# Kernel optimization log

Hardware: AMD Instinct MI355X
Metric: run time of the kernel (lower is better)

Reference implementation:

```python
import jax, jax.numpy as jnp
import numpy as np

N, E = 50000, 500000          # nodes, edges
IN_DIM, HID, OUT = 512, 256, 64  # hidden_dims = [in_dim, num_hidden, out_dim]


def setup_inputs() -> dict:
    key = jax.random.key(0)
    ks = jax.random.split(key, 6)
    features = jax.random.normal(ks[0], (N, IN_DIM), jnp.float32)
    edge_index = jax.random.randint(ks[1], (2, E), 0, N, jnp.int32)  # [src; dst]
    s1 = 1.0 / np.sqrt(IN_DIM)
    s2 = 1.0 / np.sqrt(HID)
    # torch.nn.Linear convention: weight shape (out, in), y = x @ W.T
    W1 = jax.random.uniform(ks[2], (HID, IN_DIM), jnp.float32, -s1, s1)
    W2 = jax.random.uniform(ks[3], (OUT, HID), jnp.float32, -s2, s2)
    att_src = jax.random.normal(ks[4], (HID,), jnp.float32) * 0.1
    att_dst = jax.random.normal(ks[5], (HID,), jnp.float32) * 0.1
    return dict(features=features, W1=W1, W2=W2,
                att_src=att_src, att_dst=att_dst, edge_index=edge_index)


def _gat_propagate(h, a_src, a_dst, src, dst, n):
    """STAGATE GATConv propagate: sigmoid attention logits + PyG segment softmax
    over destination nodes, then scatter-sum of weighted source features."""
    a = jax.nn.sigmoid(a_src[src] + a_dst[dst])          # [E] edge logits
    mx = jax.ops.segment_max(a, dst, num_segments=n)     # [N] per-dest max
    mx = jnp.where(jnp.isfinite(mx), mx, 0.0)            # empty segments -> 0
    e = jnp.exp(a - mx[dst])                             # [E]
    denom = jax.ops.segment_sum(e, dst, num_segments=n)  # [N]
    w = e / (denom[dst] + 1e-16)                         # [E] softmax weights
    return jax.ops.segment_sum(h[src] * w[:, None], dst, num_segments=n)


def reference(features, W1, W2, att_src, att_dst, edge_index):
    src, dst = edge_index[0], edge_index[1]
    n = features.shape[0]
    # conv1: attention=True (heads=1, concat=False)
    h1p = features @ W1.T                 # [N, HID]
    a_src = h1p @ att_src                 # [N] node-level alpha_src
    a_dst = h1p @ att_dst                 # [N] node-level alpha_dst
    h1 = jax.nn.elu(_gat_propagate(h1p, a_src, a_dst, src, dst, n))
    # conv2: attention=False -> linear only
    h2 = h1 @ W2.T                        # [N, OUT]
    # conv3: weight tied to W2.T, tied_attention = conv1's node alphas
    h3p = h2 @ W2                         # [N, HID]
    h3 = jax.nn.elu(_gat_propagate(h3p, a_src, a_dst, src, dst, n))
    # conv4: attention=False, weight tied to W1.T
    h4 = h3 @ W1                          # [N, IN_DIM]
    return h2, h4
```

## Files before the change

### kernel.cpp

```cpp
#include <hip/hip_runtime.h>
#include <hip/hip_bf16.h>

typedef unsigned short u16;
typedef unsigned int   u32;

#define N_NODES 50000
#define N_EDGES 500000
#define IN_DIM  512
#define HID     256
#define OUT_DIM 64

typedef __bf16 bf16x8 __attribute__((ext_vector_type(8)));
typedef float  f32x4  __attribute__((ext_vector_type(4)));

#define GLOBAL_AS __attribute__((address_space(1)))
#define LDS_AS    __attribute__((address_space(3)))

__device__ __forceinline__ float bf2f(u16 u) {
  union { u32 i; float f; } x; x.i = ((u32)u) << 16; return x.f;
}
__device__ __forceinline__ u16 f2bf(float f) {
  union { float f; u32 i; } x; x.f = f;
  u32 r = x.i + 0x7FFFu + ((x.i >> 16) & 1u);
  return (u16)(r >> 16);
}
__device__ __forceinline__ u32 pkbf(float a, float b) {
  return (u32)f2bf(a) | ((u32)f2bf(b) << 16);
}
__device__ __forceinline__ float lo2f(u32 w) {
  union { u32 i; float f; } x; x.i = w << 16; return x.f;
}
__device__ __forceinline__ float hi2f(u32 w) {
  union { u32 i; float f; } x; x.i = w & 0xFFFF0000u; return x.f;
}

__global__ void detect_dtype(const u32* __restrict__ feat, int* __restrict__ flag) {
  __shared__ int s[256];
  int t = threadIdx.x;
  int hits = 0;
  for (int i = t; i < 1024; i += 256) {
    u32 e = (feat[i] >> 7) & 0xFF;
    hits += (e >= 100 && e <= 140) ? 1 : 0;
  }
  s[t] = hits;
  __syncthreads();
  for (int o = 128; o > 0; o >>= 1) {
    if (t < o) s[t] += s[t + o];
    __syncthreads();
  }
  if (t == 0) *flag = (s[0] > 716) ? 1 : 0;
}

__global__ void prep(const void* __restrict__ W1r, const void* __restrict__ W2r,
                     const void* __restrict__ atsr, const void* __restrict__ atdr,
                     u16* __restrict__ W1b, u16* __restrict__ W2b,
                     u16* __restrict__ attsb, u16* __restrict__ attdb,
                     u16* __restrict__ W1T, u16* __restrict__ W2T,
                     const int* __restrict__ flag) {
  const int fv = *flag;
  int i = blockIdx.x * 256 + threadIdx.x;
  int stride = gridDim.x * 256;
  const int NW1 = HID * IN_DIM;
  const int NW2 = OUT_DIM * HID;
  for (int j = i; j < NW1; j += stride) {
    u16 v = fv ? ((const u16*)W1r)[j] : f2bf(((const float*)W1r)[j]);
    W1b[j] = v;
    int r = j >> 9, c = j & 511;
    W1T[c * HID + r] = v;
  }
  for (int j = i; j < NW2; j += stride) {
    u16 v = fv ? ((const u16*)W2r)[j] : f2bf(((const float*)W2r)[j]);
    W2b[j] = v;
    int r = j >> 8, c = j & 255;
    W2T[c * OUT_DIM + r] = v;
  }
  if (blockIdx.x == 0 && threadIdx.x < HID) {
    int t = threadIdx.x;
    attsb[t] = fv ? ((const u16*)atsr)[t] : f2bf(((const float*)atsr)[t]);
    attdb[t] = fv ? ((const u16*)atdr)[t] : f2bf(((const float*)atdr)[t]);
  }
}

__device__ __forceinline__ void glds16(const u16* g, __bf16* l) {
  __builtin_amdgcn_global_load_lds((const GLOBAL_AS u32*)g, (LDS_AS u32*)l, 16, 0, 0);
}

template <int MODE, int ABF16>
__global__ __launch_bounds__(256) void gemm128(const u16* __restrict__ A,
                                               const float* __restrict__ Af32,
                                               const u16* __restrict__ B,
                                               u16* __restrict__ Cb,
                                               void* __restrict__ outbase,
                                               size_t out_off,
                                               const u16* __restrict__ attsb,
                                               const u16* __restrict__ attdb,
                                               float* __restrict__ a_s,
                                               float* __restrict__ a_d,
                                               const int* __restrict__ flag,
                                               int M, int N, int K) {
  __shared__ __bf16 As[64 * 64];
  __shared__ __bf16 Bs[128 * 64];
  __shared__ float as_l[128];
  __shared__ float ad_l[128];

  const int fv = *flag;
  if (MODE == 3 && ABF16 != fv) return;

  const int tid  = threadIdx.x;
  const int wave = tid >> 6;
  const int lane = tid & 63;
  const int m0   = blockIdx.x * 64;
  const int n0   = blockIdx.y * 128;
  const int wm   = (wave >> 1) * 32;
  const int wn   = (wave & 1) * 64;
  const int quad = lane >> 4;
  const int l16  = lane & 15;

  if (MODE == 3 && tid < 128) {
    as_l[tid] = bf2f(attsb[n0 + tid]);
    ad_l[tid] = bf2f(attdb[n0 + tid]);
  }

  const int r8 = lane >> 3;
  const int sg = (lane & 7) ^ r8;

  const u16* bp[4];
#pragma unroll
  for (int l = 0; l < 4; ++l) {
    int br = n0 + l * 32 + wave * 8 + r8;
    bp[l] = B + (size_t)br * K + sg * 8;
  }

  const u16* ap[2];
  if (ABF16) {
#pragma unroll
    for (int l = 0; l < 2; ++l) {
      int ar = m0 + l * 32 + wave * 8 + r8;
      if (ar >= M) ar = M - 1;
      ap[l] = A + (size_t)ar * K + sg * 8;
    }
  }
  const float* afp = nullptr;
  const int rr = tid >> 2, hh = tid & 3;
  if (!ABF16) {
    int ar = m0 + rr;
    if (ar >= M) ar = M - 1;
    afp = Af32 + (size_t)ar * K + hh * 16;
  }

  f32x4 acc[2][4];
#pragma unroll
  for (int i = 0; i < 2; ++i)
#pragma unroll
    for (int j = 0; j < 4; ++j) acc[i][j] = (f32x4)0.f;

  float4 fa[4];
  if (!ABF16) {
#pragma unroll
    for (int c = 0; c < 4; ++c) fa[c] = *(const float4*)(afp + 4 * c);
  }

  for (int k0 = 0; k0 < K; k0 += 64) {
    if (ABF16) {
      __syncthreads();
#pragma unroll
      for (int l = 0; l < 2; ++l)
        glds16(ap[l] + k0, As + (l * 32 + wave * 8) * 64);
#pragma unroll
      for (int l = 0; l < 4; ++l)
        glds16(bp[l] + k0, Bs + (l * 32 + wave * 8) * 64);
      __syncthreads();
    } else {
      __builtin_amdgcn_s_barrier();
      __builtin_amdgcn_sched_barrier(0);
#pragma unroll
      for (int l = 0; l < 4; ++l)
        glds16(bp[l] + k0, Bs + (l * 32 + wave * 8) * 64);
      __builtin_amdgcn_sched_barrier(0);
#pragma unroll
      for (int j = 0; j < 2; ++j) {
        int phys = ((hh * 2 + j) ^ (rr & 7)) * 8;
        uint4 o;
        o.x = pkbf(fa[2 * j].x, fa[2 * j].y);
        o.y = pkbf(fa[2 * j].z, fa[2 * j].w);
        o.z = pkbf(fa[2 * j + 1].x, fa[2 * j + 1].y);
        o.w = pkbf(fa[2 * j + 1].z, fa[2 * j + 1].w);
        *(uint4*)&As[rr * 64 + phys] = o;
      }
      __builtin_amdgcn_sched_barrier(0);
      if (k0 + 64 < K) {
#pragma unroll
        for (int c = 0; c < 4; ++c)
          fa[c] = *(const float4*)(afp + k0 + 64 + 4 * c);
        __builtin_amdgcn_sched_barrier(0);
        asm volatile("s_waitcnt vmcnt(4) lgkmcnt(0)" ::: "memory");
      } else {
        asm volatile("s_waitcnt vmcnt(0) lgkmcnt(0)" ::: "memory");
      }
      __builtin_amdgcn_sched_barrier(0);
      __builtin_amdgcn_s_barrier();
      __builtin_amdgcn_sched_barrier(0);
    }

    bf16x8 af[2][2], bfr[4][2];
#pragma unroll
    for (int ks = 0; ks < 2; ++ks) {
#pragma unroll
      for (int mi = 0; mi < 2; ++mi)
        af[mi][ks] = *(const bf16x8*)&As[(wm + mi * 16 + l16) * 64 +
                                         (((ks * 4 + quad) ^ (l16 & 7)) * 8)];
#pragma unroll
      for (int ni = 0; ni < 4; ++ni)
        bfr[ni][ks] = *(const bf16x8*)&Bs[(wn + ni * 16 + l16) * 64 +
                                          (((ks * 4 + quad) ^ (l16 & 7)) * 8)];
    }
#pragma unroll
    for (int ks = 0; ks < 2; ++ks)
#pragma unroll
      for (int mi = 0; mi < 2; ++mi)
#pragma unroll
        for (int ni = 0; ni < 4; ++ni)
          acc[mi][ni] = __builtin_amdgcn_mfma_f32_16x16x32_bf16(
              af[mi][ks], bfr[ni][ks], acc[mi][ni], 0, 0, 0);
  }

  if (MODE == 3) {
    __syncthreads();
#pragma unroll
    for (int mi = 0; mi < 2; ++mi)
#pragma unroll
      for (int r = 0; r < 4; ++r) {
        float ps = 0.f, pd = 0.f;
#pragma unroll
        for (int ni = 0; ni < 4; ++ni) {
          int c = wn + ni * 16 + l16;
          ps += acc[mi][ni][r] * as_l[c];
          pd += acc[mi][ni][r] * ad_l[c];
        }
#pragma unroll
        for (int o = 1; o < 16; o <<= 1) {
          ps += __shfl_xor(ps, o);
          pd += __shfl_xor(pd, o);
        }
        int gr = m0 + wm + mi * 16 + quad * 4 + r;
        if (l16 == 0 && gr < M) {
          atomicAdd(&a_s[gr], ps);
          atomicAdd(&a_d[gr], pd);
        }
      }
  }

#pragma unroll
  for (int mi = 0; mi < 2; ++mi)
#pragma unroll
    for (int ni = 0; ni < 4; ++ni)
#pragma unroll
      for (int r = 0; r < 4; ++r) {
        int gr = m0 + wm + mi * 16 + quad * 4 + r;
        int gc = n0 + wn + ni * 16 + l16;
        if (gr < M) {
          float  v   = acc[mi][ni][r];
          size_t idx = (size_t)gr * N + gc;
          if (MODE == 1) {
            if (fv) ((u16*)outbase)[out_off + idx] = f2bf(v);
            else    ((float*)outbase)[out_off + idx] = v;
          } else if (MODE == 2) {
            v = (v > 0.f) ? v : expm1f(v);
            Cb[idx] = f2bf(v);
          } else {
            Cb[idx] = f2bf(v);
          }
        }
      }
}

__global__ __launch_bounds__(256) void gemm_h2(const u16* __restrict__ A,
                                               const u16* __restrict__ B,
                                               void* __restrict__ outbase,
                                               u16* __restrict__ Cb,
                                               const int* __restrict__ flag,
                                               int M, int N, int K) {
  __shared__ __bf16 As[64 * 48];
  __shared__ __bf16 Bs[64 * 48];

  const int tid  = threadIdx.x;
  const int m0   = blockIdx.x * 64;
  const int wave = tid >> 6;
  const int lane = tid & 63;
  const int wm   = (wave >> 1) * 32;
  const int wn   = (wave & 1) * 32;
  const int quad = lane >> 4;
  const int l16  = lane & 15;

  const int srow = tid >> 2;
  const int sseg = (tid & 3) * 8;
  int arow = m0 + srow;
  if (arow >= M) arow = M - 1;
  const size_t a_base = (size_t)arow * K + sseg;
  const size_t b_base = (size_t)srow * K + sseg;

  f32x4 acc[2][2];
#pragma unroll
  for (int i = 0; i < 2; ++i)
#pragma unroll
    for (int j = 0; j < 2; ++j) acc[i][j] = (f32x4)0.f;

  for (int k0 = 0; k0 < K; k0 += 32) {
    uint4 av = *(const uint4*)(A + a_base + k0);
    uint4 bv = *(const uint4*)(B + b_base + k0);
    __syncthreads();
    *(uint4*)(&As[srow * 48 + sseg]) = av;
    *(uint4*)(&Bs[srow * 48 + sseg]) = bv;
    __syncthreads();

    bf16x8 af[2], bfr[2];
#pragma unroll
    for (int mi = 0; mi < 2; ++mi)
      af[mi] = *(const bf16x8*)(&As[(wm + mi * 16 + l16) * 48 + quad * 8]);
#pragma unroll
    for (int ni = 0; ni < 2; ++ni)
      bfr[ni] = *(const bf16x8*)(&Bs[(wn + ni * 16 + l16) * 48 + quad * 8]);
#pragma unroll
    for (int mi = 0; mi < 2; ++mi)
#pragma unroll
      for (int ni = 0; ni < 2; ++ni)
        acc[mi][ni] = __builtin_amdgcn_mfma_f32_16x16x32_bf16(
            af[mi], bfr[ni], acc[mi][ni], 0, 0, 0);
  }

  const int fv = *flag;
#pragma unroll
  for (int mi = 0; mi < 2; ++mi)
#pragma unroll
    for (int ni = 0; ni < 2; ++ni)
#pragma unroll
      for (int r = 0; r < 4; ++r) {
        int gr = m0 + wm + mi * 16 + quad * 4 + r;
        int gc = wn + ni * 16 + l16;
        if (gr < M && gc < N) {
          float  v   = acc[mi][ni][r];
          size_t idx = (size_t)gr * N + gc;
          u16 bv = f2bf(v);
          if (fv) ((u16*)outbase)[idx] = bv;
          else    ((float*)outbase)[idx] = v;
          Cb[idx] = bv;
        }
      }
}

__global__ void hist_kernel(const int* __restrict__ dst, int* __restrict__ counts) {
  int e = blockIdx.x * 256 + threadIdx.x;
  if (e < N_EDGES) atomicAdd(&counts[dst[e]], 1);
}

__global__ void block_sum(const int* __restrict__ counts, int n,
                          int* __restrict__ bsums) {
  __shared__ int s[256];
  int i = blockIdx.x * 256 + threadIdx.x;
  s[threadIdx.x] = (i < n) ? counts[i] : 0;
  __syncthreads();
  for (int off = 128; off > 0; off >>= 1) {
    if (threadIdx.x < off) s[threadIdx.x] += s[threadIdx.x + off];
    __syncthreads();
  }
  if (threadIdx.x == 0) bsums[blockIdx.x] = s[0];
}

__global__ void scan_bsums(const int* __restrict__ bsums, int nb,
                           int* __restrict__ boffs) {
  __shared__ int s[256];
  int t = threadIdx.x;
  int v = (t < nb) ? bsums[t] : 0;
  s[t] = v;
  __syncthreads();
  for (int off = 1; off < 256; off <<= 1) {
    int add = (t >= off) ? s[t - off] : 0;
    __syncthreads();
    s[t] += add;
    __syncthreads();
  }
  boffs[t] = s[t] - v;
}

__global__ void scan_final(const int* __restrict__ counts,
                           const int* __restrict__ boffs, int n,
                           int* __restrict__ offsets, int* __restrict__ cursor) {
  __shared__ int s[256];
  int t = threadIdx.x;
  int i = blockIdx.x * 256 + t;
  int v = (i < n) ? counts[i] : 0;
  s[t] = v;
  __syncthreads();
  for (int off = 1; off < 256; off <<= 1) {
    int add = (t >= off) ? s[t - off] : 0;
    __syncthreads();
    s[t] += add;
    __syncthreads();
  }
  int excl = boffs[blockIdx.x] + s[t] - v;
  if (i < n) {
    offsets[i] = excl;
    cursor[i]  = excl;
  }
  if (i == n - 1) offsets[n] = excl + v;
}

__global__ void edge_scatter(const int* __restrict__ src, const int* __restrict__ dst,
                             const float* __restrict__ a_s, const float* __restrict__ a_d,
                             float* __restrict__ denom, int* __restrict__ cursor,
                             int2* __restrict__ edges) {
  int e = blockIdx.x * 256 + threadIdx.x;
  if (e >= N_EDGES) return;
  int s = src[e], d = dst[e];
  float x  = a_s[s] + a_d[d];
  float a  = 1.f / (1.f + expf(-x));
  float ev = expf(a);
  atomicAdd(&denom[d], ev);
  int pos = atomicAdd(&cursor[d], 1);
  edges[pos] = make_int2(s, __float_as_int(ev));
}

__global__ __launch_bounds__(256) void prop256(
    const int* __restrict__ offs, const int2* __restrict__ edges,
    const float* __restrict__ denom, const u16* __restrict__ feat,
    u16* __restrict__ out) {
  const int sub  = threadIdx.x >> 5;
  const int lane = threadIdx.x & 31;
  const int nd   = blockIdx.x * 8 + sub;
  const int col  = lane * 8;
  const int beg = offs[nd], end = offs[nd + 1];
  float a[8];
#pragma unroll
  for (int j = 0; j < 8; ++j) a[j] = 0.f;
  int e = beg;
  for (; e + 1 < end; e += 2) {
    int2  e0 = edges[e];
    int2  e1 = edges[e + 1];
    float v0 = __int_as_float(e0.y);
    float v1 = __int_as_float(e1.y);
    uint4 w0 = *(const uint4*)(feat + (size_t)e0.x * HID + col);
    uint4 w1 = *(const uint4*)(feat + (size_t)e1.x * HID + col);
    a[0] += v0 * lo2f(w0.x); a[1] += v0 * hi2f(w0.x);
    a[2] += v0 * lo2f(w0.y); a[3] += v0 * hi2f(w0.y);
    a[4] += v0 * lo2f(w0.z); a[5] += v0 * hi2f(w0.z);
    a[6] += v0 * lo2f(w0.w); a[7] += v0 * hi2f(w0.w);
    a[0] += v1 * lo2f(w1.x); a[1] += v1 * hi2f(w1.x);
    a[2] += v1 * lo2f(w1.y); a[3] += v1 * hi2f(w1.y);
    a[4] += v1 * lo2f(w1.z); a[5] += v1 * hi2f(w1.z);
    a[6] += v1 * lo2f(w1.w); a[7] += v1 * hi2f(w1.w);
  }
  if (e < end) {
    int2  ed = edges[e];
    float ev = __int_as_float(ed.y);
    uint4 w = *(const uint4*)(feat + (size_t)ed.x * HID + col);
    a[0] += ev * lo2f(w.x); a[1] += ev * hi2f(w.x);
    a[2] += ev * lo2f(w.y); a[3] += ev * hi2f(w.y);
    a[4] += ev * lo2f(w.z); a[5] += ev * hi2f(w.z);
    a[6] += ev * lo2f(w.w); a[7] += ev * hi2f(w.w);
  }
  float dn = 1.f / (denom[nd] + 1e-16f);
  u32 p[4];
#pragma unroll
  for (int j = 0; j < 4; ++j) {
    float r0 = a[2 * j] * dn;
    float r1 = a[2 * j + 1] * dn;
    r0 = (r0 > 0.f) ? r0 : expm1f(r0);
    r1 = (r1 > 0.f) ? r1 : expm1f(r1);
    p[j] = (u32)f2bf(r0) | ((u32)f2bf(r1) << 16);
  }
  *(uint4*)(out + (size_t)nd * HID + col) = make_uint4(p[0], p[1], p[2], p[3]);
}

__global__ __launch_bounds__(256) void prop64(
    const int* __restrict__ offs, const int2* __restrict__ edges,
    const float* __restrict__ denom, const u16* __restrict__ feat,
    u16* __restrict__ out) {
  const int sub  = threadIdx.x >> 3;
  const int lane = threadIdx.x & 7;
  const int nd   = blockIdx.x * 32 + sub;
  if (nd >= N_NODES) return;
  const int col  = lane * 8;
  const int beg = offs[nd], end = offs[nd + 1];
  float a[8];
#pragma unroll
  for (int j = 0; j < 8; ++j) a[j] = 0.f;
  int e = beg;
  for (; e + 1 < end; e += 2) {
    int2  e0 = edges[e];
    int2  e1 = edges[e + 1];
    float v0 = __int_as_float(e0.y);
    float v1 = __int_as_float(e1.y);
    uint4 w0 = *(const uint4*)(feat + (size_t)e0.x * OUT_DIM + col);
    uint4 w1 = *(const uint4*)(feat + (size_t)e1.x * OUT_DIM + col);
    a[0] += v0 * lo2f(w0.x); a[1] += v0 * hi2f(w0.x);
    a[2] += v0 * lo2f(w0.y); a[3] += v0 * hi2f(w0.y);
    a[4] += v0 * lo2f(w0.z); a[5] += v0 * hi2f(w0.z);
    a[6] += v0 * lo2f(w0.w); a[7] += v0 * hi2f(w0.w);
    a[0] += v1 * lo2f(w1.x); a[1] += v1 * hi2f(w1.x);
    a[2] += v1 * lo2f(w1.y); a[3] += v1 * hi2f(w1.y);
    a[4] += v1 * lo2f(w1.z); a[5] += v1 * hi2f(w1.z);
    a[6] += v1 * lo2f(w1.w); a[7] += v1 * hi2f(w1.w);
  }
  if (e < end) {
    int2  ed = edges[e];
    float ev = __int_as_float(ed.y);
    uint4 w = *(const uint4*)(feat + (size_t)ed.x * OUT_DIM + col);
    a[0] += ev * lo2f(w.x); a[1] += ev * hi2f(w.x);
    a[2] += ev * lo2f(w.y); a[3] += ev * hi2f(w.y);
    a[4] += ev * lo2f(w.z); a[5] += ev * hi2f(w.z);
    a[6] += ev * lo2f(w.w); a[7] += ev * hi2f(w.w);
  }
  float dn = 1.f / (denom[nd] + 1e-16f);
  u32 p[4];
#pragma unroll
  for (int j = 0; j < 4; ++j) {
    p[j] = (u32)f2bf(a[2 * j] * dn) | ((u32)f2bf(a[2 * j + 1] * dn) << 16);
  }
  *(uint4*)(out + (size_t)nd * OUT_DIM + col) = make_uint4(p[0], p[1], p[2], p[3]);
}

extern "C" void kernel_launch(void* const* d_in, const int* in_sizes, int n_in,
                              void* d_out, int out_size, void* d_ws, size_t ws_size,
                              hipStream_t stream) {
  const void* X    = d_in[0];
  const void* W1   = d_in[1];
  const void* W2   = d_in[2];
  const void* atts = d_in[3];
  const void* attd = d_in[4];
  const int*  eidx = (const int*)d_in[5];
  const int*  esrc = eidx;
  const int*  edst = eidx + N_EDGES;

  char*  ws  = (char*)d_ws;
  size_t off = 0;
  auto alloc = [&](size_t bytes) -> void* {
    void* p = ws + off;
    off += (bytes + 255) & ~(size_t)255;
    return p;
  };
  u16*   W1b    = (u16*)alloc((size_t)HID * IN_DIM * 2);
  u16*   W2b    = (u16*)alloc((size_t)OUT_DIM * HID * 2);
  u16*   attsb  = (u16*)alloc(HID * 2);
  u16*   attdb  = (u16*)alloc(HID * 2);
  u16*   W1T    = (u16*)alloc((size_t)IN_DIM * HID * 2);
  u16*   W2T    = (u16*)alloc((size_t)HID * OUT_DIM * 2);
  u16*   feat   = (u16*)alloc((size_t)N_NODES * HID * 2);
  u16*   h1     = (u16*)alloc((size_t)N_NODES * HID * 2);
  u16*   h2b    = (u16*)alloc((size_t)N_NODES * OUT_DIM * 2);
  u16*   ph2    = (u16*)alloc((size_t)N_NODES * OUT_DIM * 2);
  float* a_s    = (float*)alloc(N_NODES * 4);
  float* a_d    = (float*)alloc(N_NODES * 4);
  float* denom  = (float*)alloc(N_NODES * 4);
  int*   counts = (int*)alloc(N_NODES * 4);
  int*   offsets= (int*)alloc((N_NODES + 1) * 4);
  int*   cursor = (int*)alloc(N_NODES * 4);
  int*   bsums  = (int*)alloc(1024 * 4);
  int*   boffs  = (int*)alloc(1024 * 4);
  int2*  edges  = (int2*)alloc((size_t)N_EDGES * 8);
  int*   flag   = (int*)alloc(256);
  (void)ws_size; (void)in_sizes; (void)n_in; (void)out_size;

  size_t zero_bytes = (size_t)((char*)offsets - (char*)a_s);
  hipMemsetAsync(a_s, 0, zero_bytes, stream);

  detect_dtype<<<1, 256, 0, stream>>>((const u32*)X, flag);
  prep<<<512, 256, 0, stream>>>(W1, W2, atts, attd, W1b, W2b, attsb, attdb,
                                W1T, W2T, flag);

  const int MBG = (N_NODES + 63) / 64;

  gemm128<3, 1><<<dim3(MBG, HID / 128), 256, 0, stream>>>(
      (const u16*)X, nullptr, W1b, feat, nullptr, 0, attsb, attdb, a_s, a_d,
      flag, N_NODES, HID, IN_DIM);
  gemm128<3, 0><<<dim3(MBG, HID / 128), 256, 0, stream>>>(
      nullptr, (const float*)X, W1b, feat, nullptr, 0, attsb, attdb, a_s, a_d,
      flag, N_NODES, HID, IN_DIM);

  const int NB = (N_NODES + 255) / 256;
  hist_kernel<<<(N_EDGES + 255) / 256, 256, 0, stream>>>(edst, counts);
  block_sum<<<NB, 256, 0, stream>>>(counts, N_NODES, bsums);
  scan_bsums<<<1, 256, 0, stream>>>(bsums, NB, boffs);
  scan_final<<<NB, 256, 0, stream>>>(counts, boffs, N_NODES, offsets, cursor);
  edge_scatter<<<(N_EDGES + 255) / 256, 256, 0, stream>>>(esrc, edst, a_s, a_d,
                                                          denom, cursor, edges);

  prop256<<<N_NODES / 8, 256, 0, stream>>>(offsets, edges, denom, feat, h1);
  gemm_h2<<<dim3(MBG, 1), 256, 0, stream>>>(h1, W2b, d_out, h2b, flag,
                                            N_NODES, OUT_DIM, HID);
  prop64<<<(N_NODES + 31) / 32, 256, 0, stream>>>(offsets, edges, denom, h2b, ph2);
  gemm128<2, 1><<<dim3(MBG, HID / 128), 256, 0, stream>>>(
      ph2, nullptr, W2T, feat, nullptr, 0, nullptr, nullptr, nullptr, nullptr,
      flag, N_NODES, HID, OUT_DIM);
  gemm128<1, 1><<<dim3(MBG, IN_DIM / 128), 256, 0, stream>>>(
      feat, nullptr, W1T, nullptr, d_out, (size_t)N_NODES * OUT_DIM,
      nullptr, nullptr, nullptr, nullptr, flag, N_NODES, IN_DIM, HID);
}
```

Before: 432.6 us.

## Double-buffer LDS tiles in gemm128 to overlap global loads with MFMA

Doubles the As/Bs shared-memory tiles and turns the K loop into a two-stage software pipeline. Each step prefetches tile t+2 into the buffer just consumed while MFMAs run on the current buffer, so there is one barrier per step instead of two. The aim is to hide global-to-LDS load latency behind compute. It doubles LDS use per block (about 48KB), which may lower occupancy, and the full vmcnt(0) waits may limit how much overlap is achieved.

```diff
diff --git a/kernel.cpp b/kernel.cpp
--- a/kernel.cpp
+++ b/kernel.cpp
@@ -98,8 +98,8 @@
                                                float* __restrict__ a_d,
                                                const int* __restrict__ flag,
                                                int M, int N, int K) {
-  __shared__ __bf16 As[64 * 64];
-  __shared__ __bf16 Bs[128 * 64];
+  __shared__ __bf16 As[2][64 * 64];
+  __shared__ __bf16 Bs[2][128 * 64];
   __shared__ float as_l[128];
   __shared__ float ad_l[128];
 
@@ -154,65 +154,63 @@
 #pragma unroll
     for (int j = 0; j < 4; ++j) acc[i][j] = (f32x4)0.f;
 
+  const int nt = K >> 6;
   float4 fa[4];
+
+  if (ABF16) {
+#pragma unroll
+    for (int l = 0; l < 2; ++l)
+      glds16(ap[l], As[0] + (l * 32 + wave * 8) * 64);
+  }
+#pragma unroll
+  for (int l = 0; l < 4; ++l)
+    glds16(bp[l], Bs[0] + (l * 32 + wave * 8) * 64);
   if (!ABF16) {
 #pragma unroll
     for (int c = 0; c < 4; ++c) fa[c] = *(const float4*)(afp + 4 * c);
-  }
-
-  for (int k0 = 0; k0 < K; k0 += 64) {
+#pragma unroll
+    for (int j = 0; j < 2; ++j) {
+      int phys = ((hh * 2 + j) ^ (rr & 7)) * 8;
+      uint4 o;
+      o.x = pkbf(fa[2 * j].x, fa[2 * j].y);
+      o.y = pkbf(fa[2 * j].z, fa[2 * j].w);
+      o.z = pkbf(fa[2 * j + 1].x, fa[2 * j + 1].y);
+      o.w = pkbf(fa[2 * j + 1].z, fa[2 * j + 1].w);
+      *(uint4*)&As[0][rr * 64 + phys] = o;
+    }
+  }
+  asm volatile("s_waitcnt vmcnt(0) lgkmcnt(0)" ::: "memory");
+  __builtin_amdgcn_s_barrier();
+  if (nt > 1) {
     if (ABF16) {
-      __syncthreads();
 #pragma unroll
       for (int l = 0; l < 2; ++l)
-        glds16(ap[l] + k0, As + (l * 32 + wave * 8) * 64);
-#pragma unroll
-      for (int l = 0; l < 4; ++l)
-        glds16(bp[l] + k0, Bs + (l * 32 + wave * 8) * 64);
-      __syncthreads();
-    } else {
-      __builtin_amdgcn_s_barrier();
-      __builtin_amdgcn_sched_barrier(0);
-#pragma unroll
-      for (int l = 0; l < 4; ++l)
-        glds16(bp[l] + k0, Bs + (l * 32 + wave * 8) * 64);
-      __builtin_amdgcn_sched_barrier(0);
-#pragma unroll
-      for (int j = 0; j < 2; ++j) {
-        int phys = ((hh * 2 + j) ^ (rr & 7)) * 8;
-        uint4 o;
-        o.x = pkbf(fa[2 * j].x, fa[2 * j].y);
-        o.y = pkbf(fa[2 * j].z, fa[2 * j].w);
-        o.z = pkbf(fa[2 * j + 1].x, fa[2 * j + 1].y);
-        o.w = pkbf(fa[2 * j + 1].z, fa[2 * j + 1].w);
-        *(uint4*)&As[rr * 64 + phys] = o;
-      }
-      __builtin_amdgcn_sched_barrier(0);
-      if (k0 + 64 < K) {
-#pragma unroll
-        for (int c = 0; c < 4; ++c)
-          fa[c] = *(const float4*)(afp + k0 + 64 + 4 * c);
-        __builtin_amdgcn_sched_barrier(0);
-        asm volatile("s_waitcnt vmcnt(4) lgkmcnt(0)" ::: "memory");
-      } else {
-        asm volatile("s_waitcnt vmcnt(0) lgkmcnt(0)" ::: "memory");
-      }
-      __builtin_amdgcn_sched_barrier(0);
-      __builtin_amdgcn_s_barrier();
-      __builtin_amdgcn_sched_barrier(0);
+        glds16(ap[l] + 64, As[1] + (l * 32 + wave * 8) * 64);
     }
+#pragma unroll
+    for (int l = 0; l < 4; ++l)
+      glds16(bp[l] + 64, Bs[1] + (l * 32 + wave * 8) * 64);
+    if (!ABF16) {
+#pragma unroll
+      for (int c = 0; c < 4; ++c) fa[c] = *(const float4*)(afp + 64 + 4 * c);
+    }
+  }
+
+  for (int t = 0; t < nt; ++t) {
+    const __bf16* Asb = As[t & 1];
+    const __bf16* Bsb = Bs[t & 1];
 
     bf16x8 af[2][2], bfr[4][2];
 #pragma unroll
     for (int ks = 0; ks < 2; ++ks) {
 #pragma unroll
       for (int mi = 0; mi < 2; ++mi)
-        af[mi][ks] = *(const bf16x8*)&As[(wm + mi * 16 + l16) * 64 +
-                                         (((ks * 4 + quad) ^ (l16 & 7)) * 8)];
+        af[mi][ks] = *(const bf16x8*)&Asb[(wm + mi * 16 + l16) * 64 +
+                                          (((ks * 4 + quad) ^ (l16 & 7)) * 8)];
 #pragma unroll
       for (int ni = 0; ni < 4; ++ni)
-        bfr[ni][ks] = *(const bf16x8*)&Bs[(wn + ni * 16 + l16) * 64 +
-                                          (((ks * 4 + quad) ^ (l16 & 7)) * 8)];
+        bfr[ni][ks] = *(const bf16x8*)&Bsb[(wn + ni * 16 + l16) * 64 +
+                                           (((ks * 4 + quad) ^ (l16 & 7)) * 8)];
     }
 #pragma unroll
     for (int ks = 0; ks < 2; ++ks)
@@ -222,6 +220,39 @@
         for (int ni = 0; ni < 4; ++ni)
           acc[mi][ni] = __builtin_amdgcn_mfma_f32_16x16x32_bf16(
               af[mi][ks], bfr[ni][ks], acc[mi][ni], 0, 0, 0);
+
+    if (t + 1 < nt) {
+      if (!ABF16) {
+#pragma unroll
+        for (int j = 0; j < 2; ++j) {
+          int phys = ((hh * 2 + j) ^ (rr & 7)) * 8;
+          uint4 o;
+          o.x = pkbf(fa[2 * j].x, fa[2 * j].y);
+          o.y = pkbf(fa[2 * j].z, fa[2 * j].w);
+          o.z = pkbf(fa[2 * j + 1].x, fa[2 * j + 1].y);
+          o.w = pkbf(fa[2 * j + 1].z, fa[2 * j + 1].w);
+          *(uint4*)&As[(t + 1) & 1][rr * 64 + phys] = o;
+        }
+      }
+      asm volatile("s_waitcnt vmcnt(0) lgkmcnt(0)" ::: "memory");
+      __builtin_amdgcn_s_barrier();
+      if (t + 2 < nt) {
+        const size_t ko = (size_t)(t + 2) * 64;
+        if (ABF16) {
+#pragma unroll
+          for (int l = 0; l < 2; ++l)
+            glds16(ap[l] + ko, As[t & 1] + (l * 32 + wave * 8) * 64);
+        }
+#pragma unroll
+        for (int l = 0; l < 4; ++l)
+          glds16(bp[l] + ko, Bs[t & 1] + (l * 32 + wave * 8) * 64);
+        if (!ABF16) {
+#pragma unroll
+          for (int c = 0; c < 4; ++c)
+            fa[c] = *(const float4*)(afp + ko + 4 * c);
+        }
+      }
+    }
   }
 
   if (MODE == 3) {
```

New measurement: 437.9 us. About the same (+1.2%).
